# Performance work log

Measured on AMD Instinct MI355X. Metric: run time of the kernel, lower is better.

Reference implementation:

```python
import jax, jax.numpy as jnp
import numpy as np

SIGMA = 1.0

def setup_inputs() -> dict:
    key = jax.random.key(0)
    k1, k2, k3 = jax.random.split(key, 3)
    X_new = jax.random.normal(k1, (8192, 128), dtype=jnp.float32)
    X_train = jax.random.normal(k2, (32768, 128), dtype=jnp.float32)
    atomic_weights = jax.random.normal(k3, (32768, 1), dtype=jnp.float32)
    return {"X_new": X_new, "X_train": X_train, "atomic_weights": atomic_weights}

def reference(X_new, X_train, atomic_weights):
    x2 = jnp.sum(X_new * X_new, axis=-1, keepdims=True)            # [N_new, 1]
    y2 = jnp.sum(X_train * X_train, axis=-1)                       # [N_train]
    cross = jnp.einsum('nd,md->nm', X_new, X_train)                # [N_new, N_train]
    dist_sq = jnp.maximum(x2 + y2[None, :] - 2.0 * cross, 0.0)
    K_new = jnp.exp(-dist_sq / (2.0 * SIGMA ** 2))
    per_atom_energy = K_new @ atomic_weights                       # [N_new, 1]
    return per_atom_energy
```

## Files before the change

### kernel.cpp

```cpp
#include <hip/hip_runtime.h>
#include <stdint.h>

typedef __attribute__((ext_vector_type(4))) int i32x4;
typedef __attribute__((ext_vector_type(16))) int i32x16;
typedef __attribute__((ext_vector_type(8))) short short8;
typedef __attribute__((ext_vector_type(16))) float f32x16;

#define LOG2E 1.4426950408889634f
#define S1 16.0f
#define S1_INV 0.0625f
#define S2 4096.0f
#define K2 (1.0f / 65536.0f)

__device__ inline float fast_exp2(float x) {
#if __has_builtin(__builtin_amdgcn_exp2f)
  return __builtin_amdgcn_exp2f(x);
#else
  float r;
  asm volatile("v_exp_f32 %0, %1" : "=v"(r) : "v"(x));
  return r;
#endif
}

__device__ inline void gload16(const void* g, void* l) {
  __builtin_amdgcn_global_load_lds(
      (const __attribute__((address_space(1))) void*)g,
      (__attribute__((address_space(3))) void*)l, 16, 0, 0);
}
__device__ inline void gload4(const void* g, void* l) {
  __builtin_amdgcn_global_load_lds(
      (const __attribute__((address_space(1))) void*)g,
      (__attribute__((address_space(3))) void*)l, 4, 0, 0);
}

__device__ inline void q4(float4 v, float pre, int& hw, int& lw) {
  float xs[4] = {v.x, v.y, v.z, v.w};
  int h = 0, l = 0;
#pragma unroll
  for (int j = 0; j < 4; ++j) {
    float x = xs[j] * pre;
    float hf = rintf(fminf(fmaxf(x * S1, -127.f), 127.f));
    float rf = x - hf * S1_INV;
    float lf = rintf(fminf(fmaxf(rf * S2, -127.f), 127.f));
    h |= ((int)hf & 255) << (8 * j);
    l |= ((int)lf & 255) << (8 * j);
  }
  hw = h;
  lw = l;
}

__global__ __launch_bounds__(256) void gk_prep(
    const float* __restrict__ Xnew, const float* __restrict__ Xtr,
    const float* __restrict__ w, float* __restrict__ s,
    float* __restrict__ pref, int M, int N) {
  int row = blockIdx.x * 4 + (threadIdx.x >> 6);
  int lane = threadIdx.x & 63;
  if (row >= M + N) return;
  const float* src =
      (row < M) ? (Xtr + (size_t)row * 128) : (Xnew + (size_t)(row - M) * 128);
  float2 v = *(const float2*)(src + lane * 2);
  float ss = v.x * v.x + v.y * v.y;
#pragma unroll
  for (int o = 32; o >= 1; o >>= 1) ss += __shfl_xor(ss, o, 64);
  if (lane == 0) {
    float e = expf(-0.5f * ss);
    if (row < M)
      s[row] = e * w[row];
    else
      pref[row - M] = e;
  }
}

__global__ __launch_bounds__(256) void gk_conv_i8(const float* __restrict__ Xtr,
                                                  char* __restrict__ planes,
                                                  int M) {
  int g = blockIdx.x * 256 + threadIdx.x;
  int row = g >> 3;
  int gr = g & 7;
  if (row >= M) return;
  const float* p = Xtr + (size_t)row * 128 + gr * 16;
  int hw[4], lw[4];
#pragma unroll
  for (int i = 0; i < 4; ++i)
    q4(*(const float4*)(p + i * 4), 1.0f, hw[i], lw[i]);
  int T = row >> 5, r = row & 31;
  size_t base = (size_t)T * 8192 + (gr >> 1) * 1024 + (gr & 1) * 512 + r * 16;
  *(i32x4*)(planes + base) = (i32x4){hw[0], hw[1], hw[2], hw[3]};
  *(i32x4*)(planes + base + 4096) = (i32x4){lw[0], lw[1], lw[2], lw[3]};
}

__global__ __launch_bounds__(512, 4) void gk_main_i8(
    const float* __restrict__ Xnew, const char* __restrict__ planes,
    const float* __restrict__ s, const float* __restrict__ pref,
    float* __restrict__ out, int N, int M, int mchunk) {
  extern __shared__ char dlds[];

  const int t = threadIdx.x;
  const int l = t & 63;
  const int w = t >> 6;
  const int cl = l & 31;
  const int lk = l >> 5;

  const int n0 = blockIdx.x * 256;
  const int M0 = blockIdx.y * mchunk;
  const int iters = mchunk >> 5;
  const int T0 = M0 >> 5;

#define STAGE(tt, buf)                                                 \
  {                                                                    \
    gload16(planes + (size_t)(T0 + (tt)) * 8192 + t * 16,              \
            dlds + (buf)*8192 + t * 16);                               \
    gload4(s + M0 + (tt)*32 + l, dlds + 24576 + (buf)*256);            \
  }

  STAGE(0, 0);
  if (iters > 1) STAGE(1, 1);

  i32x4 bh[4], bl[4];
  {
    const float* pc = Xnew + (size_t)(n0 + w * 32 + cl) * 128;
#pragma unroll
    for (int kf = 0; kf < 4; ++kf) {
      const float* p = pc + kf * 32 + lk * 16;
      int hw[4], lw[4];
#pragma unroll
      for (int i = 0; i < 4; ++i)
        q4(*(const float4*)(p + i * 4), LOG2E, hw[i], lw[i]);
      bh[kf] = (i32x4){hw[0], hw[1], hw[2], hw[3]};
      bl[kf] = (i32x4){lw[0], lw[1], lw[2], lw[3]};
    }
  }

  float out0 = 0.f;

  if (iters > 1) {
    asm volatile("s_waitcnt vmcnt(2)" ::: "memory");
  } else {
    asm volatile("s_waitcnt vmcnt(0)" ::: "memory");
  }
  __builtin_amdgcn_s_barrier();

#pragma unroll 1
  for (int it = 0; it < iters; ++it) {
    __builtin_amdgcn_sched_barrier(0);

    if (it + 2 < iters) STAGE(it + 2, (it + 2) % 3);

    const char* buf = dlds + (it % 3) * 8192;
    i32x16 acc_hh = {0}, acc_m = {0};
    __builtin_amdgcn_s_setprio(1);
#pragma unroll
    for (int kf = 0; kf < 4; ++kf) {
      const char* kb = buf + kf * 1024 + lk * 512 + cl * 16;
      i32x4 ah = *(const i32x4*)(kb);
      i32x4 al = *(const i32x4*)(kb + 4096);
      acc_hh = __builtin_amdgcn_mfma_i32_32x32x32_i8(ah, bh[kf], acc_hh, 0, 0, 0);
      acc_m = __builtin_amdgcn_mfma_i32_32x32x32_i8(ah, bl[kf], acc_m, 0, 0, 0);
      acc_m = __builtin_amdgcn_mfma_i32_32x32x32_i8(al, bh[kf], acc_m, 0, 0, 0);
    }
    __builtin_amdgcn_s_setprio(0);

    const float4* sl4 = (const float4*)(dlds + 24576 + (it % 3) * 256);
#pragma unroll
    for (int q = 0; q < 4; ++q) {
      float4 sv = sl4[q * 2 + lk];
#pragma unroll
      for (int j = 0; j < 4; ++j) {
        int r = q * 4 + j;
        float c = (float)((acc_hh[r] << 8) + acc_m[r]) * K2;
        out0 += fast_exp2(c) * (&sv.x)[j];
      }
    }

    if (it + 1 < iters) {
      if (it + 2 < iters) {
        asm volatile("s_waitcnt vmcnt(2)" ::: "memory");
      } else {
        asm volatile("s_waitcnt vmcnt(0)" ::: "memory");
      }
      __builtin_amdgcn_s_barrier();
    }
  }

  out0 += __shfl_xor(out0, 32, 64);
  if (l < 32) {
    int n = n0 + w * 32 + l;
    atomicAdd(out + n, pref[n] * out0);
  }
#undef STAGE
}

__device__ inline unsigned swz_fb(unsigned off) {
  return off ^ (((off >> 8) & 7u) << 4);
}
__device__ inline void split8(float x0, float x1, float x2, float x3,
                              float x4, float x5, float x6, float x7,
                              float scale, short8& hi, short8& lo) {
  float xs[8] = {x0, x1, x2, x3, x4, x5, x6, x7};
#pragma unroll
  for (int i = 0; i < 8; ++i) {
    float v = xs[i] * scale;
    unsigned u = __float_as_uint(v);
    float hf = __uint_as_float(u & 0xffff0000u);
    float rr = v - hf;
    hi[i] = (short)(u >> 16);
    lo[i] = (short)(__float_as_uint(rr) >> 16);
  }
}

__global__ __launch_bounds__(256, 2) void gk_main_fb(
    const float* __restrict__ Xnew, const float* __restrict__ Xtr,
    const float* __restrict__ s, const float* __restrict__ pref,
    float* __restrict__ out, int N, int M, int mchunk) {
  __shared__ __attribute__((aligned(16))) char lds[33024];
  const int t = threadIdx.x;
  const int l = t & 63;
  const int w = t >> 6;
  const int lrow = l & 31;
  const int lk = l >> 5;
  const int n0 = blockIdx.x * 256;
  const int M0 = blockIdx.y * mchunk;
  const int iters = mchunk >> 6;

  short8 bh[2][8], bl[2][8];
  {
    const int colbase = n0 + w * 64;
#pragma unroll
    for (int nf = 0; nf < 2; ++nf) {
      int col = colbase + nf * 32 + lrow;
      const float* p = Xnew + (size_t)col * 128 + lk * 8;
#pragma unroll
      for (int kf = 0; kf < 8; ++kf) {
        float4 f0 = *(const float4*)(p + kf * 16);
        float4 f1 = *(const float4*)(p + kf * 16 + 4);
        split8(f0.x, f0.y, f0.z, f0.w, f1.x, f1.y, f1.z, f1.w, LOG2E,
               bh[nf][kf], bl[nf][kf]);
      }
    }
  }

  float out0 = 0.f, out1 = 0.f;
  float4 ga[4][2];
  float sreg = 0.f;
  {
    const float* abase = Xtr + (size_t)M0 * 128;
#pragma unroll
    for (int j = 0; j < 4; ++j) {
      int c = t + j * 256;
      int row = c >> 4, oct = c & 15;
      const float* p = abase + (size_t)row * 128 + oct * 8;
      ga[j][0] = *(const float4*)p;
      ga[j][1] = *(const float4*)(p + 4);
    }
    if (t < 64) sreg = s[M0 + t];
  }

#pragma unroll 1
  for (int it = 0; it < iters; ++it) {
    __syncthreads();
#pragma unroll
    for (int j = 0; j < 4; ++j) {
      int c = t + j * 256;
      int row = c >> 4, oct = c & 15;
      unsigned off = swz_fb((unsigned)(row * 256 + oct * 16));
      short8 hi, lo;
      split8(ga[j][0].x, ga[j][0].y, ga[j][0].z, ga[j][0].w, ga[j][1].x,
             ga[j][1].y, ga[j][1].z, ga[j][1].w, 1.0f, hi, lo);
      *(short8*)(lds + off) = hi;
      *(short8*)(lds + 16384 + off) = lo;
    }
    if (t < 64) *(float*)(lds + 32768 + t * 4) = sreg;
    __syncthreads();
    if (it + 1 < iters) {
      const float* abase = Xtr + (size_t)(M0 + (it + 1) * 64) * 128;
#pragma unroll
      for (int j = 0; j < 4; ++j) {
        int c = t + j * 256;
        int row = c >> 4, oct = c & 15;
        const float* p = abase + (size_t)row * 128 + oct * 8;
        ga[j][0] = *(const float4*)p;
        ga[j][1] = *(const float4*)(p + 4);
      }
      if (t < 64) sreg = s[M0 + (it + 1) * 64 + t];
    }
#pragma unroll
    for (int mf = 0; mf < 2; ++mf) {
      f32x16 acc0 = {0, 0, 0, 0, 0, 0, 0, 0, 0, 0, 0, 0, 0, 0, 0, 0};
      f32x16 acc1 = {0, 0, 0, 0, 0, 0, 0, 0, 0, 0, 0, 0, 0, 0, 0, 0};
#pragma unroll
      for (int kf = 0; kf < 8; ++kf) {
        unsigned off =
            swz_fb((unsigned)((mf * 32 + lrow) * 256 + kf * 32 + lk * 16));
        short8 ah = *(const short8*)(lds + off);
        short8 al = *(const short8*)(lds + 16384 + off);
        acc0 = __builtin_amdgcn_mfma_f32_32x32x16_bf16(ah, bh[0][kf], acc0, 0, 0, 0);
        acc1 = __builtin_amdgcn_mfma_f32_32x32x16_bf16(ah, bh[1][kf], acc1, 0, 0, 0);
        acc0 = __builtin_amdgcn_mfma_f32_32x32x16_bf16(ah, bl[0][kf], acc0, 0, 0, 0);
        acc1 = __builtin_amdgcn_mfma_f32_32x32x16_bf16(ah, bl[1][kf], acc1, 0, 0, 0);
        acc0 = __builtin_amdgcn_mfma_f32_32x32x16_bf16(al, bh[0][kf], acc0, 0, 0, 0);
        acc1 = __builtin_amdgcn_mfma_f32_32x32x16_bf16(al, bh[1][kf], acc1, 0, 0, 0);
      }
      const float* sl = (const float*)(lds + 32768 + mf * 128);
#pragma unroll
      for (int r = 0; r < 16; ++r) {
        int row = (r & 3) + 8 * (r >> 2) + 4 * lk;
        float sv = sl[row];
        out0 += fast_exp2(acc0[r]) * sv;
        out1 += fast_exp2(acc1[r]) * sv;
      }
    }
  }
  out0 += __shfl_xor(out0, 32, 64);
  out1 += __shfl_xor(out1, 32, 64);
  if (l < 32) {
    int n = n0 + w * 64 + l;
    atomicAdd(out + n, pref[n] * out0);
    n += 32;
    atomicAdd(out + n, pref[n] * out1);
  }
}

extern "C" void kernel_launch(void* const* d_in, const int* in_sizes, int n_in,
                              void* d_out, int out_size, void* d_ws,
                              size_t ws_size, hipStream_t stream) {
  const float* Xnew = (const float*)d_in[0];
  const float* Xtr = (const float*)d_in[1];
  const float* wts = (const float*)d_in[2];
  float* out = (float*)d_out;

  const int N = in_sizes[0] / 128;
  const int M = in_sizes[1] / 128;

  char* ws = (char*)d_ws;
  float* s_ws = (float*)ws;
  float* pref_ws = s_ws + M;
  char* planes_ws = ws + (size_t)(M + N) * 4;
  const size_t need = (size_t)(M + N) * 4 + (size_t)M * 256;

  hipMemsetAsync(d_out, 0, (size_t)N * sizeof(float), stream);

  int rows = M + N;
  gk_prep<<<dim3((rows + 3) / 4), 256, 0, stream>>>(Xnew, Xtr, wts, s_ws,
                                                    pref_ws, M, N);

  if (ws_size >= need) {
    gk_conv_i8<<<dim3(M * 8 / 256), 256, 0, stream>>>(Xtr, planes_ws, M);
    const int SPLIT = 16;
    dim3 grid(N / 256, SPLIT);
    gk_main_i8<<<grid, 512, 25344, stream>>>(Xnew, planes_ws, s_ws, pref_ws,
                                             out, N, M, M / SPLIT);
  } else {
    const int SPLIT = 16;
    dim3 grid(N / 256, SPLIT);
    gk_main_fb<<<grid, 256, 0, stream>>>(Xnew, Xtr, s_ws, pref_ws, out, N, M,
                                         M / SPLIT);
  }
}
```

Before: 131.2 us.

## Fuse prep into conversion/main kernels and software-pipeline MFMA with exp epilogue

Removes the separate gk_prep launch by computing training-row norms and weights inside the conversion kernel and the query-row prefactor inside the main kernel. The main loop moves to a 4-buffer LDS ring with two accumulator sets, so the MFMA for one tile is issued while the exp epilogue of the previous tile runs. This targets one kernel launch plus the serialization between matrix and transcendental work. In exchange it uses more LDS, which may lower occupancy, and more registers. The loop assumes an even tile count and clamps stage indices past the end.

New measurement: 122.4 us (median of 2 runs). 1.07x faster.

```diff
diff --git a/kernel.cpp b/kernel.cpp
--- a/kernel.cpp
+++ b/kernel.cpp
@@ -47,6 +47,161 @@
   }
   hw = h;
   lw = l;
+}
+
+__global__ __launch_bounds__(256) void gk_conv_s(const float* __restrict__ Xtr,
+                                                 const float* __restrict__ wts,
+                                                 char* __restrict__ planes,
+                                                 float* __restrict__ s, int M) {
+  int g = blockIdx.x * 256 + threadIdx.x;
+  int row = g >> 3;
+  int gr = g & 7;
+  if (row >= M) return;
+  const float* p = Xtr + (size_t)row * 128 + gr * 16;
+  int hw[4], lw[4];
+  float ss = 0.f;
+#pragma unroll
+  for (int i = 0; i < 4; ++i) {
+    float4 v = *(const float4*)(p + i * 4);
+    ss += v.x * v.x + v.y * v.y + v.z * v.z + v.w * v.w;
+    q4(v, 1.0f, hw[i], lw[i]);
+  }
+  ss += __shfl_xor(ss, 1, 64);
+  ss += __shfl_xor(ss, 2, 64);
+  ss += __shfl_xor(ss, 4, 64);
+  if (gr == 0) s[row] = expf(-0.5f * ss) * wts[row];
+
+  int T = row >> 5, r = row & 31;
+  size_t base = (size_t)T * 8192 + (gr >> 1) * 1024 + (gr & 1) * 512 + r * 16;
+  *(i32x4*)(planes + base) = (i32x4){hw[0], hw[1], hw[2], hw[3]};
+  *(i32x4*)(planes + base + 4096) = (i32x4){lw[0], lw[1], lw[2], lw[3]};
+}
+
+__global__ __launch_bounds__(512, 4) void gk_main_i8(
+    const float* __restrict__ Xnew, const char* __restrict__ planes,
+    const float* __restrict__ s, float* __restrict__ out, int N, int M,
+    int mchunk) {
+  extern __shared__ char dlds[];
+
+  const int t = threadIdx.x;
+  const int l = t & 63;
+  const int w = t >> 6;
+  const int cl = l & 31;
+  const int lk = l >> 5;
+
+  const int n0 = blockIdx.x * 256;
+  const int M0 = blockIdx.y * mchunk;
+  const int iters = mchunk >> 5;
+  const int T0 = M0 >> 5;
+
+#define STAGE(tt)                                                       \
+  {                                                                     \
+    int st_ = ((tt) < iters) ? (tt) : (iters - 1);   \
+    gload16(planes + (size_t)(T0 + st_) * 8192 + t * 16,                \
+            dlds + ((tt)&3) * 8192 + t * 16);                           \
+    gload4(s + M0 + st_ * 32 + l, dlds + 32768 + ((tt)&3) * 256);       \
+  }
+
+#define COMPUTE(acc_hh, acc_m, tile)                                    \
+  {                                                                     \
+    const char* buf_ = dlds + ((tile)&3) * 8192;                        \
+    acc_hh = zero16;                                                    \
+    acc_m = zero16;                                                     \
+    __builtin_amdgcn_s_setprio(1);                                      \
+    _Pragma("unroll") for (int kf = 0; kf < 4; ++kf) {                  \
+      const char* kb_ = buf_ + kf * 1024 + lk * 512 + cl * 16;          \
+      i32x4 ah_ = *(const i32x4*)(kb_);                                 \
+      i32x4 al_ = *(const i32x4*)(kb_ + 4096);                          \
+      acc_hh = __builtin_amdgcn_mfma_i32_32x32x32_i8(ah_, bh[kf], acc_hh, 0, 0, 0); \
+      acc_m = __builtin_amdgcn_mfma_i32_32x32x32_i8(ah_, bl[kf], acc_m, 0, 0, 0);   \
+      acc_m = __builtin_amdgcn_mfma_i32_32x32x32_i8(al_, bh[kf], acc_m, 0, 0, 0);   \
+    }                                                                   \
+    __builtin_amdgcn_s_setprio(0);                                      \
+  }
+
+#define EPI(acc_hh, acc_m, tile)                                        \
+  {                                                                     \
+    const float4* sl4_ =                                                \
+        (const float4*)(dlds + 32768 + ((tile)&3) * 256);               \
+    _Pragma("unroll") for (int q = 0; q < 4; ++q) {                     \
+      float4 sv_ = sl4_[q * 2 + lk];                                    \
+      _Pragma("unroll") for (int j = 0; j < 4; ++j) {                   \
+        int r_ = q * 4 + j;                                             \
+        float c_ = (float)((acc_hh[r_] << 8) + acc_m[r_]) * K2;         \
+        out0 += fast_exp2(c_) * (&sv_.x)[j];                            \
+      }                                                                 \
+    }                                                                   \
+  }
+
+  const i32x16 zero16 = {0, 0, 0, 0, 0, 0, 0, 0, 0, 0, 0, 0, 0, 0, 0, 0};
+
+  STAGE(0);
+  STAGE(1);
+
+  i32x4 bh[4], bl[4];
+  float pref;
+  {
+    float ss = 0.f;
+    const float* pc = Xnew + (size_t)(n0 + w * 32 + cl) * 128;
+#pragma unroll
+    for (int kf = 0; kf < 4; ++kf) {
+      const float* p = pc + kf * 32 + lk * 16;
+      int hw[4], lw[4];
+#pragma unroll
+      for (int i = 0; i < 4; ++i) {
+        float4 v = *(const float4*)(p + i * 4);
+        ss += v.x * v.x + v.y * v.y + v.z * v.z + v.w * v.w;
+        q4(v, LOG2E, hw[i], lw[i]);
+      }
+      bh[kf] = (i32x4){hw[0], hw[1], hw[2], hw[3]};
+      bl[kf] = (i32x4){lw[0], lw[1], lw[2], lw[3]};
+    }
+    ss += __shfl_xor(ss, 32, 64);
+    pref = expf(-0.5f * ss);
+  }
+
+  float out0 = 0.f;
+  i32x16 hhA, mA, hhB, mB;
+
+  asm volatile("s_waitcnt vmcnt(2)" ::: "memory");
+  __builtin_amdgcn_s_barrier();
+
+  __builtin_amdgcn_sched_barrier(0);
+  STAGE(2);
+  COMPUTE(hhA, mA, 0);
+  asm volatile("s_waitcnt vmcnt(2)" ::: "memory");
+  __builtin_amdgcn_s_barrier();
+
+#pragma unroll 1
+  for (int tt = 1; tt < iters - 1; tt += 2) {
+    __builtin_amdgcn_sched_barrier(0);
+    STAGE(tt + 2);
+    COMPUTE(hhB, mB, tt);
+    EPI(hhA, mA, tt - 1);
+    asm volatile("s_waitcnt vmcnt(2)" ::: "memory");
+    __builtin_amdgcn_s_barrier();
+
+    __builtin_amdgcn_sched_barrier(0);
+    STAGE(tt + 3);
+    COMPUTE(hhA, mA, tt + 1);
+    EPI(hhB, mB, tt);
+    asm volatile("s_waitcnt vmcnt(2)" ::: "memory");
+    __builtin_amdgcn_s_barrier();
+  }
+
+  __builtin_amdgcn_sched_barrier(0);
+  COMPUTE(hhB, mB, iters - 1);
+  EPI(hhA, mA, iters - 2);
+  EPI(hhB, mB, iters - 1);
+
+  out0 += __shfl_xor(out0, 32, 64);
+  if (l < 32) {
+    int n = n0 + w * 32 + l;
+    atomicAdd(out + n, pref * out0);
+  }
+#undef STAGE
+#undef COMPUTE
+#undef EPI
 }
 
 __global__ __launch_bounds__(256) void gk_prep(
@@ -69,125 +224,6 @@
     else
       pref[row - M] = e;
   }
-}
-
-__global__ __launch_bounds__(256) void gk_conv_i8(const float* __restrict__ Xtr,
-                                                  char* __restrict__ planes,
-                                                  int M) {
-  int g = blockIdx.x * 256 + threadIdx.x;
-  int row = g >> 3;
-  int gr = g & 7;
-  if (row >= M) return;
-  const float* p = Xtr + (size_t)row * 128 + gr * 16;
-  int hw[4], lw[4];
-#pragma unroll
-  for (int i = 0; i < 4; ++i)
-    q4(*(const float4*)(p + i * 4), 1.0f, hw[i], lw[i]);
-  int T = row >> 5, r = row & 31;
-  size_t base = (size_t)T * 8192 + (gr >> 1) * 1024 + (gr & 1) * 512 + r * 16;
-  *(i32x4*)(planes + base) = (i32x4){hw[0], hw[1], hw[2], hw[3]};
-  *(i32x4*)(planes + base + 4096) = (i32x4){lw[0], lw[1], lw[2], lw[3]};
-}
-
-__global__ __launch_bounds__(512, 4) void gk_main_i8(
-    const float* __restrict__ Xnew, const char* __restrict__ planes,
-    const float* __restrict__ s, const float* __restrict__ pref,
-    float* __restrict__ out, int N, int M, int mchunk) {
-  extern __shared__ char dlds[];
-
-  const int t = threadIdx.x;
-  const int l = t & 63;
-  const int w = t >> 6;
-  const int cl = l & 31;
-  const int lk = l >> 5;
-
-  const int n0 = blockIdx.x * 256;
-  const int M0 = blockIdx.y * mchunk;
-  const int iters = mchunk >> 5;
-  const int T0 = M0 >> 5;
-
-#define STAGE(tt, buf)                                                 \
-  {                                                                    \
-    gload16(planes + (size_t)(T0 + (tt)) * 8192 + t * 16,              \
-            dlds + (buf)*8192 + t * 16);                               \
-    gload4(s + M0 + (tt)*32 + l, dlds + 24576 + (buf)*256);            \
-  }
-
-  STAGE(0, 0);
-  if (iters > 1) STAGE(1, 1);
-
-  i32x4 bh[4], bl[4];
-  {
-    const float* pc = Xnew + (size_t)(n0 + w * 32 + cl) * 128;
-#pragma unroll
-    for (int kf = 0; kf < 4; ++kf) {
-      const float* p = pc + kf * 32 + lk * 16;
-      int hw[4], lw[4];
-#pragma unroll
-      for (int i = 0; i < 4; ++i)
-        q4(*(const float4*)(p + i * 4), LOG2E, hw[i], lw[i]);
-      bh[kf] = (i32x4){hw[0], hw[1], hw[2], hw[3]};
-      bl[kf] = (i32x4){lw[0], lw[1], lw[2], lw[3]};
-    }
-  }
-
-  float out0 = 0.f;
-
-  if (iters > 1) {
-    asm volatile("s_waitcnt vmcnt(2)" ::: "memory");
-  } else {
-    asm volatile("s_waitcnt vmcnt(0)" ::: "memory");
-  }
-  __builtin_amdgcn_s_barrier();
-
-#pragma unroll 1
-  for (int it = 0; it < iters; ++it) {
-    __builtin_amdgcn_sched_barrier(0);
-
-    if (it + 2 < iters) STAGE(it + 2, (it + 2) % 3);
-
-    const char* buf = dlds + (it % 3) * 8192;
-    i32x16 acc_hh = {0}, acc_m = {0};
-    __builtin_amdgcn_s_setprio(1);
-#pragma unroll
-    for (int kf = 0; kf < 4; ++kf) {
-      const char* kb = buf + kf * 1024 + lk * 512 + cl * 16;
-      i32x4 ah = *(const i32x4*)(kb);
-      i32x4 al = *(const i32x4*)(kb + 4096);
-      acc_hh = __builtin_amdgcn_mfma_i32_32x32x32_i8(ah, bh[kf], acc_hh, 0, 0, 0);
-      acc_m = __builtin_amdgcn_mfma_i32_32x32x32_i8(ah, bl[kf], acc_m, 0, 0, 0);
-      acc_m = __builtin_amdgcn_mfma_i32_32x32x32_i8(al, bh[kf], acc_m, 0, 0, 0);
-    }
-    __builtin_amdgcn_s_setprio(0);
-
-    const float4* sl4 = (const float4*)(dlds + 24576 + (it % 3) * 256);
-#pragma unroll
-    for (int q = 0; q < 4; ++q) {
-      float4 sv = sl4[q * 2 + lk];
-#pragma unroll
-      for (int j = 0; j < 4; ++j) {
-        int r = q * 4 + j;
-        float c = (float)((acc_hh[r] << 8) + acc_m[r]) * K2;
-        out0 += fast_exp2(c) * (&sv.x)[j];
-      }
-    }
-
-    if (it + 1 < iters) {
-      if (it + 2 < iters) {
-        asm volatile("s_waitcnt vmcnt(2)" ::: "memory");
-      } else {
-        asm volatile("s_waitcnt vmcnt(0)" ::: "memory");
-      }
-      __builtin_amdgcn_s_barrier();
-    }
-  }
-
-  out0 += __shfl_xor(out0, 32, 64);
-  if (l < 32) {
-    int n = n0 + w * 32 + l;
-    atomicAdd(out + n, pref[n] * out0);
-  }
-#undef STAGE
 }
 
 __device__ inline unsigned swz_fb(unsigned off) {
@@ -333,23 +369,23 @@
 
   char* ws = (char*)d_ws;
   float* s_ws = (float*)ws;
-  float* pref_ws = s_ws + M;
-  char* planes_ws = ws + (size_t)(M + N) * 4;
-  const size_t need = (size_t)(M + N) * 4 + (size_t)M * 256;
+  char* planes_ws = ws + (size_t)M * 4;
+  const size_t need = (size_t)M * 4 + (size_t)M * 256;
 
   hipMemsetAsync(d_out, 0, (size_t)N * sizeof(float), stream);
 
-  int rows = M + N;
-  gk_prep<<<dim3((rows + 3) / 4), 256, 0, stream>>>(Xnew, Xtr, wts, s_ws,
-                                                    pref_ws, M, N);
-
   if (ws_size >= need) {
-    gk_conv_i8<<<dim3(M * 8 / 256), 256, 0, stream>>>(Xtr, planes_ws, M);
+    gk_conv_s<<<dim3(M * 8 / 256), 256, 0, stream>>>(Xtr, wts, planes_ws,
+                                                     s_ws, M);
     const int SPLIT = 16;
     dim3 grid(N / 256, SPLIT);
-    gk_main_i8<<<grid, 512, 25344, stream>>>(Xnew, planes_ws, s_ws, pref_ws,
-                                             out, N, M, M / SPLIT);
+    gk_main_i8<<<grid, 512, 33792, stream>>>(Xnew, planes_ws, s_ws, out, N, M,
+                                             M / SPLIT);
   } else {
+    float* pref_ws = s_ws + M;
+    int rows = M + N;
+    gk_prep<<<dim3((rows + 3) / 4), 256, 0, stream>>>(Xnew, Xtr, wts, s_ws,
+                                                      pref_ws, M, N);
     const int SPLIT = 16;
     dim3 grid(N / 256, SPLIT);
     gk_main_fb<<<grid, 256, 0, stream>>>(Xnew, Xtr, s_ws, pref_ws, out, N, M,
```
